# Performance work log

Hardware: AMD Instinct MI355X
Metric: run time of the kernel (lower is better)

Reference implementation:

```python
import jax, jax.numpy as jnp
import numpy as np


def _ens_linear(x, W, b):
    # x: [B,T,Din], W: [E,Din,Dout], b: [E,Dout] -> [E,B,T,Dout]
    return jnp.einsum('btd,edh->ebth', x, W) + b[:, None, None, :]


def _gilr_scan(v, f):
    # h_t = f_t * h_{t-1} + (1 - f_t) * v_t, h_0 = 0 (tie-input-gate linear recurrence)
    def comb(c1, c2):
        a1, b1 = c1
        a2, b2 = c2
        return a2 * a1, a2 * b1 + b2
    _, h = jax.lax.associative_scan(comb, (f, (1.0 - f) * v), axis=1)
    return h


def setup_inputs() -> dict:
    key = jax.random.key(0)
    ks = jax.random.split(key, 7)
    B, T, Din, D = 8, 4096, 512, 512
    x = jax.random.normal(ks[0], (B, T, Din), dtype=jnp.float32)
    s_in = 1.0 / np.sqrt(Din)
    s = 1.0 / np.sqrt(D)
    W_in = jax.random.uniform(ks[1], (2, Din, D), jnp.float32, -s_in, s_in)
    b_in = jax.random.uniform(ks[2], (2, D), jnp.float32, -s_in, s_in)
    W_mid = jax.random.uniform(ks[3], (4, D, D), jnp.float32, -s, s)
    b_mid = jax.random.uniform(ks[4], (4, D), jnp.float32, -s, s)
    W_out = jax.random.uniform(ks[5], (D, D), jnp.float32, -s, s)
    b_out = jax.random.uniform(ks[6], (D,), jnp.float32, -s, s)
    return {"x": x, "W_in": W_in, "b_in": b_in, "W_mid": W_mid,
            "b_mid": b_mid, "W_out": W_out, "b_out": b_out}


def reference(x, W_in, b_in, W_mid, b_mid, W_out, b_out):
    # in_proj (ensemble of 2): u[0] -> v, u[1] -> f
    u = _ens_linear(x, W_in, b_in)
    v = jnp.tanh(u[0])
    f = jax.nn.sigmoid(u[1])
    # first gated linear recurrence (hidden_pre starts at zeros)
    v = _gilr_scan(v, f)
    hidden_pre = v[:, -1:, :]
    # middle_proj (ensemble of 4): f, i, o, z
    u = _ens_linear(v, W_mid, b_mid)
    f2 = jax.nn.sigmoid(u[0])
    i = jax.nn.sigmoid(u[1])
    o = jax.nn.sigmoid(u[2])
    z = jnp.tanh(u[3])
    # second gated linear recurrence (hidden_middle starts at zeros)
    out = _gilr_scan(i * z, f2)
    hidden_middle = out[:, -1:, :]
    out = out * o
    out = out @ W_out + b_out
    hidden = jnp.concatenate((hidden_pre, hidden_middle), axis=-1)
    hidden = jnp.transpose(hidden, (1, 0, 2))  # [1, B, 2D]
    return out, hidden
```

## Files before the change

kernel.cpp:

```cpp
#include <hip/hip_runtime.h>

typedef short short8 __attribute__((ext_vector_type(8)));
typedef float float4v __attribute__((ext_vector_type(4)));
typedef unsigned short u16;
typedef unsigned int u32;

#define T_LEN 4096
#define DDIM 512
#define BATCH 8
#define MROWS 32768
#define CH 32
#define NC 128

__device__ __forceinline__ u16 f2b(float x) {
    unsigned u = __float_as_uint(x);
    unsigned r = (u + 0x7FFFu + ((u >> 16) & 1u)) >> 16;
    return (u16)r;
}
__device__ __forceinline__ float b2f(u16 h) {
    return __uint_as_float((u32)h << 16);
}
__device__ __forceinline__ float sigm(float x) {
    return __builtin_amdgcn_rcpf(1.f + __builtin_amdgcn_exp2f(-1.44269504f * x));
}
__device__ __forceinline__ float tanh_fast(float x) {
    return 1.f - 2.f * __builtin_amdgcn_rcpf(1.f + __builtin_amdgcn_exp2f(2.88539008f * x));
}

__device__ __forceinline__ void gl2lds16(const u16* g, u16* l) {
    __builtin_amdgcn_global_load_lds(
        (const __attribute__((address_space(1))) void*)g,
        (__attribute__((address_space(3))) void*)l, 16, 0, 0);
}

__device__ __forceinline__ void compose_xor(float& A, float& B, int mask,
                                            bool selfIsHi) {
    float pa = __shfl_xor(A, mask);
    float pb = __shfl_xor(B, mask);
    float loA = selfIsHi ? pa : A, loB = selfIsHi ? pb : B;
    float hiA = selfIsHi ? A : pa, hiB = selfIsHi ? B : pb;
    A = hiA * loA;
    B = hiA * loB + hiB;
}

__global__ __launch_bounds__(256) void cvt_x(const float* __restrict__ x,
                                             u16* __restrict__ xb, size_t n) {
    size_t i = ((size_t)blockIdx.x * 256 + threadIdx.x) * 4;
    if (i < n) {
        float4v v = *(const float4v*)&x[i];
        ushort4 p;
        p.x = f2b(v[0]); p.y = f2b(v[1]); p.z = f2b(v[2]); p.w = f2b(v[3]);
        *(ushort4*)&xb[i] = p;
    }
}

__global__ __launch_bounds__(256) void cvt_wt_all(
    const float* __restrict__ W_in, const float* __restrict__ W_mid,
    const float* __restrict__ W_out, u16* __restrict__ wt_in,
    u16* __restrict__ wt_mid, u16* __restrict__ wt_out) {
    int idx = blockIdx.x * 256 + threadIdx.x;
    int j = idx >> 9;
    int k = idx & 511;
    if (j < 1024) {
        int gate = (j >> 4) & 1, d = (j >> 5) * 16 + (j & 15);
        wt_in[(size_t)j * 512 + k] =
            f2b(W_in[((size_t)gate * 512 + k) * 512 + d]);
    } else if (j < 3072) {
        int j2 = j - 1024;
        int gate = (j2 >> 4) & 3, d = (j2 >> 6) * 16 + (j2 & 15);
        wt_mid[(size_t)j2 * 512 + k] =
            f2b(W_mid[((size_t)gate * 512 + k) * 512 + d]);
    } else {
        int j3 = j - 3072;
        wt_out[(size_t)j3 * 512 + k] = f2b(W_out[(size_t)k * 512 + j3]);
    }
}

template <int MODE>
__global__ __launch_bounds__(512, 4) void gemm_act(
    const u16* __restrict__ A, const u16* __restrict__ Bt,
    const float* __restrict__ bias, void* __restrict__ o0v,
    void* __restrict__ o1v, void* __restrict__ o2v,
    float* __restrict__ cA, float* __restrict__ cB) {
    constexpr int K = 512;
    constexpr int BK = 32;
    constexpr int NKT = K / BK;
    constexpr int LBA = 256 * 32;
    constexpr int LBB = 128 * 32;
    constexpr int GX = (MODE == 1) ? 8 : (MODE == 2) ? 16 : 4;
    constexpr int NWG = 128 * GX;
    __shared__ u16 lsA[3][LBA];
    __shared__ u16 lsB[3][LBB];
    const int tid = threadIdx.x;
    const int lane = tid & 63;
    const int wid = tid >> 6;
    const int wr = wid >> 1;
    const int wc = wid & 1;
    const int l0 = lane & 15, lh = lane >> 4;

    const int h = blockIdx.x;
    const int l = (h & 7) * (NWG / 8) + (h >> 3);
    const int bn0 = (l & (GX - 1)) * 128;
    const int bm0 = (l / GX) * 256;

    float4v acc[4][4];
#pragma unroll
    for (int m = 0; m < 4; ++m)
#pragma unroll
        for (int n = 0; n < 4; ++n) acc[m][n] = (float4v){0.f, 0.f, 0.f, 0.f};

    int growA[2], gchA[2], growB, gchB;
#pragma unroll
    for (int i = 0; i < 2; ++i) {
        int flat = i * 512 + tid;
        growA[i] = flat >> 2;
        gchA[i] = (((flat & 3) ^ ((growA[i] >> 1) & 3))) * 8;
    }
    growB = tid >> 2;
    gchB = (((tid & 3) ^ ((growB >> 1) & 3))) * 8;

#define STAGE(buf, kt)                                                        \
    {                                                                         \
        const int k0 = (kt) * BK;                                             \
        _Pragma("unroll") for (int i = 0; i < 2; ++i)                         \
            gl2lds16(&A[(size_t)(bm0 + growA[i]) * K + k0 + gchA[i]],         \
                     &lsA[buf][(i * 512 + tid) * 8]);                         \
        gl2lds16(&Bt[(size_t)(bn0 + growB) * K + k0 + gchB],                  \
                 &lsB[buf][tid * 8]);                                         \
    }

    STAGE(0, 0);
    STAGE(1, 1);

    for (int kt = 0; kt < NKT; ++kt) {
        const int cur = kt % 3;
        if (kt + 1 < NKT)
            asm volatile("s_waitcnt vmcnt(3)" ::: "memory");
        else
            asm volatile("s_waitcnt vmcnt(0)" ::: "memory");
        __builtin_amdgcn_s_barrier();
        __builtin_amdgcn_sched_barrier(0);
        if (kt + 2 < NKT) STAGE((kt + 2) % 3, kt + 2);
        short8 af[4], bf[4];
#pragma unroll
        for (int m = 0; m < 4; ++m) {
            int r = wr * 64 + m * 16 + l0;
            af[m] = *(const short8*)&lsA[cur][r * 32 + ((lh ^ ((r >> 1) & 3)) * 8)];
        }
#pragma unroll
        for (int n = 0; n < 4; ++n) {
            int r = wc * 64 + n * 16 + l0;
            bf[n] = *(const short8*)&lsB[cur][r * 32 + ((lh ^ ((r >> 1) & 3)) * 8)];
        }
        asm volatile("s_waitcnt lgkmcnt(0)" ::: "memory");
        __builtin_amdgcn_sched_barrier(0);
        __builtin_amdgcn_s_setprio(1);
#pragma unroll
        for (int m = 0; m < 4; ++m)
#pragma unroll
            for (int n = 0; n < 4; ++n)
                acc[m][n] = __builtin_amdgcn_mfma_f32_16x16x32_bf16(
                    af[m], bf[n], acc[m][n], 0, 0, 0);
        __builtin_amdgcn_s_setprio(0);
    }
#undef STAGE

    if (MODE == 3) {
#pragma unroll
        for (int m = 0; m < 4; ++m) {
#pragma unroll
            for (int n = 0; n < 4; ++n) {
                int col = bn0 + wc * 64 + n * 16 + l0;
                float bv = bias[col];
#pragma unroll
                for (int r = 0; r < 4; ++r) {
                    int rw = bm0 + wr * 64 + m * 16 + lh * 4 + r;
                    ((float*)o0v)[(size_t)rw * 512 + col] = acc[m][n][r] + bv;
                }
            }
        }
        return;
    }

    const int bb = bm0 >> 12;
    const int tq = (bm0 & 4095) + wr * 64;

    if (MODE == 1) {
        const int base5 = (bn0 + wc * 64) >> 5;
#pragma unroll
        for (int p = 0; p < 2; ++p) {
            const int d = (base5 + p) * 16 + l0;
            const float bvv = bias[d], bvf = bias[512 + d];
            float segA[4], segB[4];
#pragma unroll
            for (int m = 0; m < 4; ++m) {
                float Ap = 1.f, Bp = 0.f;
#pragma unroll
                for (int r = 0; r < 4; ++r) {
                    int rw = bm0 + wr * 64 + m * 16 + lh * 4 + r;
                    float f1 = sigm(acc[m][2 * p + 1][r] + bvf);
                    float g = (1.f - f1) * tanh_fast(acc[m][2 * p][r] + bvv);
                    size_t oidx = (size_t)rw * 512 + d;
                    ((u16*)o0v)[oidx] = f2b(f1);
                    ((u16*)o1v)[oidx] = f2b(g);
                    Bp = f1 * Bp + g;
                    Ap *= f1;
                }
                segA[m] = Ap; segB[m] = Bp;
            }
#pragma unroll
            for (int m = 0; m < 4; ++m) {
                compose_xor(segA[m], segB[m], 16, (lh & 1) != 0);
                compose_xor(segA[m], segB[m], 32, (lh & 2) != 0);
            }
            if (lh == 0) {
                float c0A = segA[1] * segA[0], c0B = segA[1] * segB[0] + segB[1];
                float c1A = segA[3] * segA[2], c1B = segA[3] * segB[2] + segB[3];
                int c0 = tq >> 5;
                size_t ci0 = (size_t)c0 * 4096 + bb * 512 + d;
                size_t ci1 = ci0 + 4096;
                cA[ci0] = c0A; cB[ci0] = c0B;
                cA[ci1] = c1A; cB[ci1] = c1B;
            }
        }
    } else {
        const int d = ((bn0 + wc * 64) >> 6) * 16 + l0;
        const float bv0 = bias[d], bv1 = bias[512 + d];
        const float bv2 = bias[1024 + d], bv3 = bias[1536 + d];
        float segA[4], segB[4];
#pragma unroll
        for (int m = 0; m < 4; ++m) {
            float Ap = 1.f, Bp = 0.f;
#pragma unroll
            for (int r = 0; r < 4; ++r) {
                int rw = bm0 + wr * 64 + m * 16 + lh * 4 + r;
                float f2 = sigm(acc[m][0][r] + bv0);
                float ii = sigm(acc[m][1][r] + bv1);
                float oo = sigm(acc[m][2][r] + bv2);
                float zz = tanh_fast(acc[m][3][r] + bv3);
                float g = (1.f - f2) * ii * zz;
                size_t oidx = (size_t)rw * 512 + d;
                ((u16*)o0v)[oidx] = f2b(f2);
                ((u16*)o1v)[oidx] = f2b(g);
                ((u16*)o2v)[oidx] = f2b(oo);
                Bp = f2 * Bp + g;
                Ap *= f2;
            }
            segA[m] = Ap; segB[m] = Bp;
        }
#pragma unroll
        for (int m = 0; m < 4; ++m) {
            compose_xor(segA[m], segB[m], 16, (lh & 1) != 0);
            compose_xor(segA[m], segB[m], 32, (lh & 2) != 0);
        }
        if (lh == 0) {
            float c0A = segA[1] * segA[0], c0B = segA[1] * segB[0] + segB[1];
            float c1A = segA[3] * segA[2], c1B = segA[3] * segB[2] + segB[3];
            int c0 = tq >> 5;
            size_t ci0 = (size_t)c0 * 4096 + bb * 512 + d;
            size_t ci1 = ci0 + 4096;
            cA[ci0] = c0A; cB[ci0] = c0B;
            cA[ci1] = c1A; cB[ci1] = c1B;
        }
    }
}

__global__ __launch_bounds__(256) void scan_p2(float* __restrict__ cA,
                                               const float* __restrict__ cB) {
    int ln = blockIdx.x * 256 + threadIdx.x;
    float h = 0.f;
    for (int c = 0; c < NC; ++c) {
        size_t ix = (size_t)c * 4096 + ln;
        float a = cA[ix], bb = cB[ix];
        cA[ix] = h;
        h = a * h + bb;
    }
}

template <int S>
__global__ __launch_bounds__(128) void scan_p3(
    const u16* __restrict__ f, const u16* __restrict__ g,
    const u16* __restrict__ o, const float* __restrict__ cA,
    u16* __restrict__ hb, float* __restrict__ hid) {
    int d0 = threadIdx.x * 4;
    int c = blockIdx.x & (NC - 1);
    int b = blockIdx.x >> 7;
    size_t base = ((size_t)b * T_LEN + c * CH) * DDIM + d0;
    size_t ci = (size_t)c * 4096 + b * DDIM + d0;
    float h[4] = {cA[ci], cA[ci + 1], cA[ci + 2], cA[ci + 3]};
    for (int t = 0; t < CH; ++t) {
        ushort4 fq = *(const ushort4*)&f[base];
        ushort4 gq = *(const ushort4*)&g[base];
        float ff[4] = {b2f(fq.x), b2f(fq.y), b2f(fq.z), b2f(fq.w)};
        float gg[4] = {b2f(gq.x), b2f(gq.y), b2f(gq.z), b2f(gq.w)};
        float w[4];
#pragma unroll
        for (int j = 0; j < 4; ++j) {
            h[j] = ff[j] * h[j] + gg[j];
            w[j] = h[j];
        }
        if (S == 2) {
            ushort4 oq = *(const ushort4*)&o[base];
            w[0] *= b2f(oq.x); w[1] *= b2f(oq.y);
            w[2] *= b2f(oq.z); w[3] *= b2f(oq.w);
        }
        ushort4 p;
        p.x = f2b(w[0]); p.y = f2b(w[1]); p.z = f2b(w[2]); p.w = f2b(w[3]);
        *(ushort4*)&hb[base] = p;
        base += DDIM;
    }
    if (c == NC - 1) {
#pragma unroll
        for (int j = 0; j < 4; ++j)
            hid[b * 1024 + (S == 1 ? 0 : 512) + d0 + j] = h[j];
    }
}

extern "C" void kernel_launch(void* const* d_in, const int* in_sizes, int n_in,
                              void* d_out, int out_size, void* d_ws,
                              size_t ws_size, hipStream_t stream) {
    const float* x = (const float*)d_in[0];
    const float* W_in = (const float*)d_in[1];
    const float* b_in = (const float*)d_in[2];
    const float* W_mid = (const float*)d_in[3];
    const float* b_mid = (const float*)d_in[4];
    const float* W_out = (const float*)d_in[5];
    const float* b_out = (const float*)d_in[6];
    float* out = (float*)d_out;
    char* ws = (char*)d_ws;

    const size_t MB = 1u << 20;
    const size_t MD = (size_t)MROWS * DDIM;

    u16* wt_in = (u16*)(ws);
    u16* wt_mid = (u16*)(ws + 1 * MB);
    u16* wt_out = (u16*)(ws + 3 * MB);
    u16* hb = (u16*)(ws + 4 * MB);
    u16* S0 = (u16*)(ws + 36 * MB);
    u16* S1 = (u16*)(ws + 68 * MB);
    u16* S2 = (u16*)(ws + 100 * MB);
    float* cA = (float*)(ws + 164 * MB);
    float* cB = (float*)(ws + 166 * MB);
    float* hid = out + MD;

    cvt_x<<<(int)(MD / 4 / 256), 256, 0, stream>>>(x, hb, MD);
    cvt_wt_all<<<7168, 256, 0, stream>>>(W_in, W_mid, W_out, wt_in, wt_mid,
                                         wt_out);

    gemm_act<1><<<1024, 512, 0, stream>>>(hb, wt_in, b_in, S0, S1, nullptr,
                                          cA, cB);
    scan_p2<<<16, 256, 0, stream>>>(cA, cB);
    scan_p3<1><<<1024, 128, 0, stream>>>(S0, S1, nullptr, cA, hb, hid);

    gemm_act<2><<<2048, 512, 0, stream>>>(hb, wt_mid, b_mid, S0, S1, S2,
                                          cA, cB);
    scan_p2<<<16, 256, 0, stream>>>(cA, cB);
    scan_p3<2><<<1024, 128, 0, stream>>>(S0, S1, S2, cA, hb, hid);

    gemm_act<3><<<512, 512, 0, stream>>>(hb, wt_out, b_out, out, nullptr,
                                         nullptr, nullptr, nullptr);
}
```

Baseline: 238.9 us.

## Fuse carry-prefix into scan and fuse second scan with output GEMM

Drops the serial scan_p2 kernel. Each scan block now recomputes its own carry-in by folding all earlier chunk summaries from cA/cB. The second scan is fused into a new output-projection GEMM: the gated output tile is written to LDS in bf16 and multiplied by W_out with MFMA directly, so the hb round trip and the separate MODE 3 GEMM launch go away. The cost is redundant prefix work (up to 127 chunk loads per block), B fragments read straight from global memory with only register double-buffering, and lower occupancy from 64KB of LDS per block.

```diff
diff --git a/kernel.cpp b/kernel.cpp
--- a/kernel.cpp
+++ b/kernel.cpp
@@ -87,7 +87,7 @@
     constexpr int NKT = K / BK;
     constexpr int LBA = 256 * 32;
     constexpr int LBB = 128 * 32;
-    constexpr int GX = (MODE == 1) ? 8 : (MODE == 2) ? 16 : 4;
+    constexpr int GX = (MODE == 1) ? 8 : 16;
     constexpr int NWG = 128 * GX;
     __shared__ u16 lsA[3][LBA];
     __shared__ u16 lsB[3][LBB];
@@ -164,23 +164,6 @@
         __builtin_amdgcn_s_setprio(0);
     }
 #undef STAGE
-
-    if (MODE == 3) {
-#pragma unroll
-        for (int m = 0; m < 4; ++m) {
-#pragma unroll
-            for (int n = 0; n < 4; ++n) {
-                int col = bn0 + wc * 64 + n * 16 + l0;
-                float bv = bias[col];
-#pragma unroll
-                for (int r = 0; r < 4; ++r) {
-                    int rw = bm0 + wr * 64 + m * 16 + lh * 4 + r;
-                    ((float*)o0v)[(size_t)rw * 512 + col] = acc[m][n][r] + bv;
-                }
-            }
-        }
-        return;
-    }
 
     const int bb = bm0 >> 12;
     const int tq = (bm0 & 4095) + wr * 64;
@@ -265,54 +248,147 @@
     }
 }
 
-__global__ __launch_bounds__(256) void scan_p2(float* __restrict__ cA,
-                                               const float* __restrict__ cB) {
-    int ln = blockIdx.x * 256 + threadIdx.x;
-    float h = 0.f;
-    for (int c = 0; c < NC; ++c) {
-        size_t ix = (size_t)c * 4096 + ln;
-        float a = cA[ix], bb = cB[ix];
-        cA[ix] = h;
-        h = a * h + bb;
-    }
-}
-
-template <int S>
-__global__ __launch_bounds__(128) void scan_p3(
+__global__ __launch_bounds__(128) void scan_p3_1(
     const u16* __restrict__ f, const u16* __restrict__ g,
-    const u16* __restrict__ o, const float* __restrict__ cA,
+    const float* __restrict__ cA, const float* __restrict__ cB,
     u16* __restrict__ hb, float* __restrict__ hid) {
     int d0 = threadIdx.x * 4;
     int c = blockIdx.x & (NC - 1);
     int b = blockIdx.x >> 7;
+    float h[4] = {0.f, 0.f, 0.f, 0.f};
+    for (int cp = 0; cp < c; ++cp) {
+        size_t ix = (size_t)cp * 4096 + b * DDIM + d0;
+        float4v a = *(const float4v*)&cA[ix];
+        float4v bb = *(const float4v*)&cB[ix];
+#pragma unroll
+        for (int j = 0; j < 4; ++j) h[j] = a[j] * h[j] + bb[j];
+    }
     size_t base = ((size_t)b * T_LEN + c * CH) * DDIM + d0;
-    size_t ci = (size_t)c * 4096 + b * DDIM + d0;
-    float h[4] = {cA[ci], cA[ci + 1], cA[ci + 2], cA[ci + 3]};
     for (int t = 0; t < CH; ++t) {
         ushort4 fq = *(const ushort4*)&f[base];
         ushort4 gq = *(const ushort4*)&g[base];
         float ff[4] = {b2f(fq.x), b2f(fq.y), b2f(fq.z), b2f(fq.w)};
         float gg[4] = {b2f(gq.x), b2f(gq.y), b2f(gq.z), b2f(gq.w)};
-        float w[4];
-#pragma unroll
-        for (int j = 0; j < 4; ++j) {
-            h[j] = ff[j] * h[j] + gg[j];
-            w[j] = h[j];
-        }
-        if (S == 2) {
-            ushort4 oq = *(const ushort4*)&o[base];
-            w[0] *= b2f(oq.x); w[1] *= b2f(oq.y);
-            w[2] *= b2f(oq.z); w[3] *= b2f(oq.w);
-        }
+#pragma unroll
+        for (int j = 0; j < 4; ++j) h[j] = ff[j] * h[j] + gg[j];
         ushort4 p;
-        p.x = f2b(w[0]); p.y = f2b(w[1]); p.z = f2b(w[2]); p.w = f2b(w[3]);
+        p.x = f2b(h[0]); p.y = f2b(h[1]); p.z = f2b(h[2]); p.w = f2b(h[3]);
         *(ushort4*)&hb[base] = p;
         base += DDIM;
     }
     if (c == NC - 1) {
 #pragma unroll
-        for (int j = 0; j < 4; ++j)
-            hid[b * 1024 + (S == 1 ? 0 : 512) + d0 + j] = h[j];
+        for (int j = 0; j < 4; ++j) hid[b * 1024 + d0 + j] = h[j];
+    }
+}
+
+__global__ __launch_bounds__(256) void scan_gemm3(
+    const u16* __restrict__ f, const u16* __restrict__ g,
+    const u16* __restrict__ o, const float* __restrict__ cA,
+    const float* __restrict__ cB, const u16* __restrict__ Wt,
+    const float* __restrict__ bias, float* __restrict__ out,
+    float* __restrict__ hid) {
+    __shared__ u16 lds_s[64 * 512];
+    const int tid = threadIdx.x;
+
+    const int hh = blockIdx.x;
+    const int lg = (hh & 7) * 64 + (hh >> 3);
+    const int b = lg >> 6, c2 = lg & 63;
+
+    {
+        const int ccl = tid >> 7;
+        const int d0 = (tid & 127) * 4;
+        const int cc = c2 * 2 + ccl;
+        float h[4] = {0.f, 0.f, 0.f, 0.f};
+        for (int cp = 0; cp < cc; ++cp) {
+            size_t ix = (size_t)cp * 4096 + b * DDIM + d0;
+            float4v a = *(const float4v*)&cA[ix];
+            float4v bb = *(const float4v*)&cB[ix];
+#pragma unroll
+            for (int j = 0; j < 4; ++j) h[j] = a[j] * h[j] + bb[j];
+        }
+        size_t base = ((size_t)b * T_LEN + cc * CH) * DDIM + d0;
+        const int cd = d0 >> 3, dlo = d0 & 7;
+        for (int t = 0; t < CH; ++t) {
+            ushort4 fq = *(const ushort4*)&f[base];
+            ushort4 gq = *(const ushort4*)&g[base];
+            ushort4 oq = *(const ushort4*)&o[base];
+            float ff[4] = {b2f(fq.x), b2f(fq.y), b2f(fq.z), b2f(fq.w)};
+            float gg[4] = {b2f(gq.x), b2f(gq.y), b2f(gq.z), b2f(gq.w)};
+            float oo[4] = {b2f(oq.x), b2f(oq.y), b2f(oq.z), b2f(oq.w)};
+            float w[4];
+#pragma unroll
+            for (int j = 0; j < 4; ++j) {
+                h[j] = ff[j] * h[j] + gg[j];
+                w[j] = h[j] * oo[j];
+            }
+            int row = ccl * 32 + t;
+            ushort4 p;
+            p.x = f2b(w[0]); p.y = f2b(w[1]); p.z = f2b(w[2]); p.w = f2b(w[3]);
+            *(ushort4*)&lds_s[row * 512 + ((cd ^ (row & 7)) << 3) + dlo] = p;
+            base += DDIM;
+        }
+        if (cc == NC - 1) {
+#pragma unroll
+            for (int j = 0; j < 4; ++j) hid[b * 1024 + 512 + d0 + j] = h[j];
+        }
+    }
+    __syncthreads();
+
+    const int lane = tid & 63;
+    const int wid = tid >> 6;
+    const int l0 = lane & 15, lh = lane >> 4;
+
+    float4v acc[4][8];
+#pragma unroll
+    for (int m = 0; m < 4; ++m)
+#pragma unroll
+        for (int n = 0; n < 8; ++n) acc[m][n] = (float4v){0.f, 0.f, 0.f, 0.f};
+
+    const u16* wbase = &Wt[(size_t)(wid * 128 + l0) * 512 + lh * 8];
+
+    short8 bfc[8], bfn[8];
+#pragma unroll
+    for (int n = 0; n < 8; ++n)
+        bfc[n] = *(const short8*)&wbase[(size_t)n * 16 * 512];
+
+    for (int ks = 0; ks < 16; ++ks) {
+        if (ks < 15) {
+#pragma unroll
+            for (int n = 0; n < 8; ++n)
+                bfn[n] = *(const short8*)&wbase[(size_t)n * 16 * 512 +
+                                                (ks + 1) * 32];
+        }
+        short8 af[4];
+#pragma unroll
+        for (int m = 0; m < 4; ++m) {
+            int row = m * 16 + l0;
+            int cd = (ks * 4 + lh) ^ (row & 7);
+            af[m] = *(const short8*)&lds_s[row * 512 + cd * 8];
+        }
+#pragma unroll
+        for (int m = 0; m < 4; ++m)
+#pragma unroll
+            for (int n = 0; n < 8; ++n)
+                acc[m][n] = __builtin_amdgcn_mfma_f32_16x16x32_bf16(
+                    af[m], bfc[n], acc[m][n], 0, 0, 0);
+#pragma unroll
+        for (int n = 0; n < 8; ++n) bfc[n] = bfn[n];
+    }
+
+    const size_t rbase = (size_t)b * T_LEN + c2 * 64;
+#pragma unroll
+    for (int m = 0; m < 4; ++m) {
+#pragma unroll
+        for (int n = 0; n < 8; ++n) {
+            int col = wid * 128 + n * 16 + l0;
+            float bv = bias[col];
+#pragma unroll
+            for (int r = 0; r < 4; ++r) {
+                size_t rw = rbase + m * 16 + lh * 4 + r;
+                out[rw * 512 + col] = acc[m][n][r] + bv;
+            }
+        }
     }
 }
 
@@ -349,14 +425,10 @@
 
     gemm_act<1><<<1024, 512, 0, stream>>>(hb, wt_in, b_in, S0, S1, nullptr,
                                           cA, cB);
-    scan_p2<<<16, 256, 0, stream>>>(cA, cB);
-    scan_p3<1><<<1024, 128, 0, stream>>>(S0, S1, nullptr, cA, hb, hid);
+    scan_p3_1<<<1024, 128, 0, stream>>>(S0, S1, cA, cB, hb, hid);
 
     gemm_act<2><<<2048, 512, 0, stream>>>(hb, wt_mid, b_mid, S0, S1, S2,
                                           cA, cB);
-    scan_p2<<<16, 256, 0, stream>>>(cA, cB);
-    scan_p3<2><<<1024, 128, 0, stream>>>(S0, S1, S2, cA, hb, hid);
-
-    gemm_act<3><<<512, 512, 0, stream>>>(hb, wt_out, b_out, out, nullptr,
-                                         nullptr, nullptr, nullptr);
-}
+    scan_gemm3<<<512, 256, 0, stream>>>(S0, S1, S2, cA, cB, wt_out, b_out,
+                                        out, hid);
+}
```

Measured after the change: 300.8 us. 1.26x slower.
